# Kernel optimization log

Hardware: AMD Instinct MI355X
Metric: run time of the kernel (lower is better)

## Reference

```python
import jax, jax.numpy as jnp
import numpy as np

NR, NS, GS, APP_DIM = 4096, 128, 128, 27
FEAPE, VIEWPE, FC = 6, 6, 128
IN_MLPC = APP_DIM + 3 + 2 * FEAPE * APP_DIM + 2 * VIEWPE * 3  # 390
DENSITY_SHIFT, DIST_SCALE = -10.0, 25.0


def positional_encoding(x, freqs):
    # matches torch: (x[..., None] * 2**k).reshape(..., freqs*dim), then [sin, cos]
    fb = 2.0 ** jnp.arange(freqs, dtype=x.dtype)
    p = (x[..., None] * fb).reshape(x.shape[:-1] + (freqs * x.shape[-1],))
    return jnp.concatenate([jnp.sin(p), jnp.cos(p)], axis=-1)


def grid_sample3d(vol, coords):
    # vol: [C, D, H, W]; coords: [N, 3] xyz in [-1, 1] (x->W, y->H, z->D)
    # trilinear, align_corners=True (matches F.grid_sample)
    C, D, H, W = vol.shape

    def axis(c, S):
        i = (c + 1.0) * 0.5 * (S - 1)
        i0 = jnp.clip(jnp.floor(i), 0, S - 2).astype(jnp.int32)
        return i0, i - i0

    x0, wx = axis(coords[:, 0], W)
    y0, wy = axis(coords[:, 1], H)
    z0, wz = axis(coords[:, 2], D)

    def g(zi, yi, xi):
        return vol[:, zi, yi, xi]  # [C, N]

    c00 = g(z0, y0, x0) * (1 - wx) + g(z0, y0, x0 + 1) * wx
    c01 = g(z0, y0 + 1, x0) * (1 - wx) + g(z0, y0 + 1, x0 + 1) * wx
    c10 = g(z0 + 1, y0, x0) * (1 - wx) + g(z0 + 1, y0, x0 + 1) * wx
    c11 = g(z0 + 1, y0 + 1, x0) * (1 - wx) + g(z0 + 1, y0 + 1, x0 + 1) * wx
    c0 = c00 * (1 - wy) + c01 * wy
    c1 = c10 * (1 - wy) + c11 * wy
    return (c0 * (1 - wz) + c1 * wz).T  # [N, C]


def setup_inputs() -> dict:
    key = jax.random.key(0)
    ks = jax.random.split(key, 12)
    xyz = jax.random.uniform(ks[0], (NR, NS, 3), jnp.float32, -1.0, 1.0)
    viewdirs = jax.random.normal(ks[1], (NR, 3), jnp.float32)
    viewdirs = viewdirs / jnp.linalg.norm(viewdirs, axis=-1, keepdims=True)
    dists = jax.random.uniform(ks[2], (NR, NS), jnp.float32, 0.0, 0.02)
    density_grid = jax.random.normal(ks[3], (1, GS, GS, GS), jnp.float32) * 3.0 + 8.0
    app_grid = jax.random.normal(ks[4], (APP_DIM, GS, GS, GS), jnp.float32) * 0.1
    w1 = jax.random.normal(ks[5], (IN_MLPC, FC), jnp.float32) / np.sqrt(IN_MLPC)
    b1 = jnp.zeros((FC,), jnp.float32)
    w2 = jax.random.normal(ks[6], (FC, FC), jnp.float32) / np.sqrt(FC)
    b2 = jnp.zeros((FC,), jnp.float32)
    w3 = jax.random.normal(ks[7], (FC, 3), jnp.float32) / np.sqrt(FC)
    b3 = jnp.zeros((3,), jnp.float32)
    return {"xyz": xyz, "viewdirs": viewdirs, "dists": dists,
            "density_grid": density_grid, "app_grid": app_grid,
            "w1": w1, "b1": b1, "w2": w2, "b2": b2, "w3": w3, "b3": b3}


def reference(xyz, viewdirs, dists, density_grid, app_grid, w1, b1, w2, b2, w3, b3):
    nr, ns, _ = xyz.shape
    pts = xyz.reshape(-1, 3)

    # density feature lookup + softplus feature2density (fea2denseAct='softplus')
    sigma_feat = grid_sample3d(density_grid, pts)[:, 0].reshape(nr, ns)
    sigma = jax.nn.softplus(sigma_feat + DENSITY_SHIFT)

    # raw2alpha: alpha compositing with transmittance cumprod
    alpha = 1.0 - jnp.exp(-sigma * dists * DIST_SCALE)  # [nr, ns]
    T = jnp.cumprod(jnp.concatenate(
        [jnp.ones((nr, 1), alpha.dtype), 1.0 - alpha + 1e-10], axis=-1), axis=-1)
    weights = alpha * T[:, :-1]  # [nr, ns]

    # appearance feature lookup + MLPRender_Fea shading
    feats = grid_sample3d(app_grid, pts)  # [nr*ns, 27]
    vdirs = jnp.broadcast_to(viewdirs[:, None, :], (nr, ns, 3)).reshape(-1, 3)
    mlp_in = jnp.concatenate(
        [feats, vdirs,
         positional_encoding(feats, FEAPE),
         positional_encoding(vdirs, VIEWPE)], axis=-1)  # [nr*ns, 390]
    h = jax.nn.relu(mlp_in @ w1 + b1)
    h = jax.nn.relu(h @ w2 + b2)
    rgb = jax.nn.sigmoid(h @ w3 + b3).reshape(nr, ns, 3)

    rgb_map = jnp.sum(weights[..., None] * rgb, axis=1)  # [nr, 3]
    return rgb_map
```

## Files before the change

kernel.cpp:

```cpp
#include <hip/hip_runtime.h>
#include <math.h>

#define NRAYS  4096
#define NSAMP  128
#define GSZ    128
#define VOX    (GSZ*GSZ*GSZ)
#define APPC   27
#define FCH    128
#define INW    390
#define K1PAD  416
#define TP     32
#define SIP    424
#define H1S    136
#define H2S    132
#define VOXPAD 32

typedef __attribute__((ext_vector_type(8))) short bf16x8;
typedef __attribute__((ext_vector_type(4))) float f32x4;

#define MFMA16(a, b, c) __builtin_amdgcn_mfma_f32_16x16x32_bf16((a), (b), (c), 0, 0, 0)

__device__ inline ushort f2b(float f) {
    union { float f; unsigned u; } x; x.f = f;
    unsigned u = x.u;
    u = (u + 0x7FFFu + ((u >> 16) & 1u)) >> 16;
    return (ushort)u;
}
__device__ inline float b2f(ushort h) {
    return __uint_as_float(((unsigned)h) << 16);
}

__global__ __launch_bounds__(256)
void transpose_app(const float* __restrict__ ag, ushort* __restrict__ out)
{
    const int v = blockIdx.x * 256 + threadIdx.x;
    ushort h[VOXPAD];
    #pragma unroll
    for (int c = 0; c < APPC; c++)
        h[c] = f2b(ag[(size_t)c * VOX + v]);
    #pragma unroll
    for (int c = APPC; c < VOXPAD; c++) h[c] = 0;
    uint4* o = reinterpret_cast<uint4*>(out + (size_t)v * VOXPAD);
    #pragma unroll
    for (int i = 0; i < 4; i++) {
        uint4 q;
        q.x = (unsigned)h[8*i+0] | ((unsigned)h[8*i+1] << 16);
        q.y = (unsigned)h[8*i+2] | ((unsigned)h[8*i+3] << 16);
        q.z = (unsigned)h[8*i+4] | ((unsigned)h[8*i+5] << 16);
        q.w = (unsigned)h[8*i+6] | ((unsigned)h[8*i+7] << 16);
        o[i] = q;
    }
}

__device__ inline bf16x8 load_b_frag(const float* __restrict__ W, int ld,
                                     int kbase, int n, int kmax)
{
    union { uint4 u; bf16x8 v; } cv;
    unsigned* pr = &cv.u.x;
    #pragma unroll
    for (int q = 0; q < 4; q++) {
        const int ka = kbase + 2*q, kb = ka + 1;
        const float fa = (ka < kmax) ? W[ka*ld + n] : 0.f;
        const float fb = (kb < kmax) ? W[kb*ld + n] : 0.f;
        pr[q] = (unsigned)f2b(fa) | ((unsigned)f2b(fb) << 16);
    }
    return cv.v;
}

__global__ __launch_bounds__(256)
void nerf_render_mfma(const float* __restrict__ xyz,
                      const float* __restrict__ viewdirs,
                      const float* __restrict__ dists,
                      const float* __restrict__ dgrid,
                      const ushort* __restrict__ agridT,
                      const float* __restrict__ w1,
                      const float* __restrict__ b1,
                      const float* __restrict__ w2,
                      const float* __restrict__ b2,
                      const float* __restrict__ w3,
                      const float* __restrict__ b3,
                      float* __restrict__ out)
{
    __shared__ __align__(16) ushort S_in[TP][SIP];
    __shared__ __align__(16) ushort s_h1[TP][H1S];
    __shared__ float  s_h2[TP][H2S];
    __shared__ int    s_base[NSAMP];
    __shared__ float  s_w8[NSAMP][8];
    __shared__ float  s_wts[NSAMP];
    __shared__ ushort s_vrow[40];
    __shared__ float  s_partial[TP*3];
    __shared__ float  s_scanw0;

    const int r    = blockIdx.x;
    const int t    = threadIdx.x;
    const int lane = t & 63;

    for (int i = t; i < TP*SIP/2; i += 256)
        reinterpret_cast<unsigned*>(&S_in[0][0])[i] = 0u;
    if (t < TP*3) s_partial[t] = 0.f;

    {
        const int s = t & 127;
        const float px = xyz[(r*NSAMP + s)*3 + 0];
        const float py = xyz[(r*NSAMP + s)*3 + 1];
        const float pz = xyz[(r*NSAMP + s)*3 + 2];
        float fx = (px + 1.0f) * 63.5f;
        float fy = (py + 1.0f) * 63.5f;
        float fz = (pz + 1.0f) * 63.5f;
        int x0 = (int)floorf(fx); x0 = min(max(x0, 0), GSZ-2);
        int y0 = (int)floorf(fy); y0 = min(max(y0, 0), GSZ-2);
        int z0 = (int)floorf(fz); z0 = min(max(z0, 0), GSZ-2);
        float wx = fx - (float)x0, wy = fy - (float)y0, wz = fz - (float)z0;
        float ux = 1.f - wx, uy = 1.f - wy, uz = 1.f - wz;
        int base = (z0*GSZ + y0)*GSZ + x0;
        float w000 = uz*uy*ux, w001 = uz*uy*wx, w010 = uz*wy*ux, w011 = uz*wy*wx;
        float w100 = wz*uy*ux, w101 = wz*uy*wx, w110 = wz*wy*ux, w111 = wz*wy*wx;
        if (t < 128) {
            s_base[s] = base;
            s_w8[s][0] = w000; s_w8[s][1] = w001; s_w8[s][2] = w010; s_w8[s][3] = w011;
            s_w8[s][4] = w100; s_w8[s][5] = w101; s_w8[s][6] = w110; s_w8[s][7] = w111;
        }
        const float* dg = dgrid + base;
        float dsum = w000*dg[0]            + w001*dg[1]
                   + w010*dg[GSZ]          + w011*dg[GSZ+1]
                   + w100*dg[GSZ*GSZ]      + w101*dg[GSZ*GSZ+1]
                   + w110*dg[GSZ*GSZ+GSZ]  + w111*dg[GSZ*GSZ+GSZ+1];
        float sf    = dsum - 10.0f;
        float sigma = fmaxf(sf, 0.f) + log1pf(expf(-fabsf(sf)));
        float alpha = 1.f - expf(-sigma * dists[r*NSAMP + s] * 25.0f);
        float v     = 1.f - alpha + 1e-10f;

        float scan = v;
        #pragma unroll
        for (int off = 1; off < 64; off <<= 1) {
            float o = __shfl_up(scan, off, 64);
            if (lane >= off) scan *= o;
        }
        if ((t & 127) == 63) s_scanw0 = scan;
        __syncthreads();
        float prev = __shfl_up(scan, 1, 64);
        float excl;
        if ((t & 127) < 64) excl = (lane == 0) ? 1.0f     : prev;
        else                excl = (lane == 0) ? s_scanw0 : prev * s_scanw0;
        if (t < 128) s_wts[s] = alpha * excl;
    }

    if (t < 21) {
        if (t < 3) {
            s_vrow[t] = f2b(viewdirs[r*3 + t]);
        } else {
            int i = t - 3;
            int d = i / 6, f = i - 6*d;
            float vd = viewdirs[r*3 + d];
            float sv, cv;
            sincosf(vd * (float)(1 << f), &sv, &cv);
            s_vrow[3  + i] = f2b(sv);
            s_vrow[21 + i] = f2b(cv);
        }
    }
    __syncthreads();

    for (int s0 = 0; s0 < NSAMP; s0 += TP) {
        {
            const int p   = t >> 3;
            const int tap = t & 7;
            const int s   = s0 + p;
            const int dz  = tap >> 2, dy = (tap >> 1) & 1, dx = tap & 1;
            const int vox = s_base[s] + dz*GSZ*GSZ + dy*GSZ + dx;
            const float wt = s_w8[s][tap];
            const ushort* vp = agridT + (size_t)vox * VOXPAD;
            const uint4 a0 = *reinterpret_cast<const uint4*>(vp);
            const uint4 a1 = *reinterpret_cast<const uint4*>(vp + 8);
            const uint4 a2 = *reinterpret_cast<const uint4*>(vp + 16);
            const uint2 a3 = *reinterpret_cast<const uint2*>(vp + 24);
            unsigned dw[14] = {a0.x,a0.y,a0.z,a0.w, a1.x,a1.y,a1.z,a1.w,
                               a2.x,a2.y,a2.z,a2.w, a3.x,a3.y};
            float f[27];
            #pragma unroll
            for (int i = 0; i < 14; i++) {
                f[2*i] = __uint_as_float(dw[i] << 16) * wt;
                if (2*i + 1 < 27)
                    f[2*i+1] = __uint_as_float(dw[i] & 0xffff0000u) * wt;
            }
            #pragma unroll
            for (int m = 1; m < 8; m <<= 1) {
                #pragma unroll
                for (int c = 0; c < 27; c++)
                    f[c] += __shfl_xor(f[c], m, 64);
            }
            #pragma unroll
            for (int c = 0; c < APPC; c++)
                if ((c & 7) == tap) S_in[p][c] = f2b(f[c]);
        }
        for (int idx = t; idx < TP*39; idx += 256) {
            int p = idx / 39, j = idx - p*39;
            S_in[p][(j < 3) ? (27 + j) : (351 + j)] = s_vrow[j];
        }
        __syncthreads();

        for (int idx = t; idx < TP*162; idx += 256) {
            int p   = idx / 162;
            int rem = idx - p*162;
            int d = rem / 6, f = rem - 6*d;
            float v = b2f(S_in[p][d]);
            float sv, cv;
            __sincosf(v * (float)(1 << f), &sv, &cv);
            S_in[p][30  + rem] = f2b(sv);
            S_in[p][192 + rem] = f2b(cv);
        }
        __syncthreads();

        const int wv = t >> 6;
        const int mt = wv & 1, nq = wv >> 1;
        const int arow  = mt*16 + (lane & 15);
        const int kg    = (lane >> 4) * 8;
        const int ncol  = lane & 15;
        const int mbase = mt*16 + (lane >> 4)*4;

        {
            f32x4 acc0 = {0.f,0.f,0.f,0.f}, acc1 = {0.f,0.f,0.f,0.f};
            f32x4 acc2 = {0.f,0.f,0.f,0.f}, acc3 = {0.f,0.f,0.f,0.f};
            const int n0 = (nq*4+0)*16 + ncol, n1 = (nq*4+1)*16 + ncol;
            const int n2 = (nq*4+2)*16 + ncol, n3 = (nq*4+3)*16 + ncol;
            for (int ks = 0; ks < 13; ks++) {
                const int k0 = ks*32 + kg;
                bf16x8 a = *reinterpret_cast<const bf16x8*>(&S_in[arow][k0]);
                acc0 = MFMA16(a, load_b_frag(w1, FCH, k0, n0, INW), acc0);
                acc1 = MFMA16(a, load_b_frag(w1, FCH, k0, n1, INW), acc1);
                acc2 = MFMA16(a, load_b_frag(w1, FCH, k0, n2, INW), acc2);
                acc3 = MFMA16(a, load_b_frag(w1, FCH, k0, n3, INW), acc3);
            }
            const float bn0 = b1[n0], bn1 = b1[n1], bn2 = b1[n2], bn3 = b1[n3];
            #pragma unroll
            for (int q = 0; q < 4; q++) {
                s_h1[mbase + q][n0] = f2b(fmaxf(acc0[q] + bn0, 0.f));
                s_h1[mbase + q][n1] = f2b(fmaxf(acc1[q] + bn1, 0.f));
                s_h1[mbase + q][n2] = f2b(fmaxf(acc2[q] + bn2, 0.f));
                s_h1[mbase + q][n3] = f2b(fmaxf(acc3[q] + bn3, 0.f));
            }
        }
        __syncthreads();

        {
            f32x4 acc0 = {0.f,0.f,0.f,0.f}, acc1 = {0.f,0.f,0.f,0.f};
            f32x4 acc2 = {0.f,0.f,0.f,0.f}, acc3 = {0.f,0.f,0.f,0.f};
            const int n0 = (nq*4+0)*16 + ncol, n1 = (nq*4+1)*16 + ncol;
            const int n2 = (nq*4+2)*16 + ncol, n3 = (nq*4+3)*16 + ncol;
            #pragma unroll
            for (int ks = 0; ks < 4; ks++) {
                const int k0 = ks*32 + kg;
                bf16x8 a = *reinterpret_cast<const bf16x8*>(&s_h1[arow][k0]);
                acc0 = MFMA16(a, load_b_frag(w2, FCH, k0, n0, FCH), acc0);
                acc1 = MFMA16(a, load_b_frag(w2, FCH, k0, n1, FCH), acc1);
                acc2 = MFMA16(a, load_b_frag(w2, FCH, k0, n2, FCH), acc2);
                acc3 = MFMA16(a, load_b_frag(w2, FCH, k0, n3, FCH), acc3);
            }
            const float bn0 = b2[n0], bn1 = b2[n1], bn2 = b2[n2], bn3 = b2[n3];
            #pragma unroll
            for (int q = 0; q < 4; q++) {
                s_h2[mbase + q][n0] = fmaxf(acc0[q] + bn0, 0.f);
                s_h2[mbase + q][n1] = fmaxf(acc1[q] + bn1, 0.f);
                s_h2[mbase + q][n2] = fmaxf(acc2[q] + bn2, 0.f);
                s_h2[mbase + q][n3] = fmaxf(acc3[q] + bn3, 0.f);
            }
        }
        __syncthreads();

        if (t < TP*3) {
            int p = t / 3, c = t - 3*p;
            float acc = b3[c];
            for (int k = 0; k < FCH; k++)
                acc = fmaf(s_h2[p][k], w3[k*3 + c], acc);
            float rgb = 1.0f / (1.0f + expf(-acc));
            s_partial[t] += s_wts[s0 + p] * rgb;
        }
        __syncthreads();
    }

    if (t < 3) {
        float sum = 0.f;
        #pragma unroll
        for (int p = 0; p < TP; p++) sum += s_partial[p*3 + t];
        out[r*3 + t] = sum;
    }
}

__global__ __launch_bounds__(128)
void nerf_render_f32(const float* __restrict__ xyz,
                     const float* __restrict__ viewdirs,
                     const float* __restrict__ dists,
                     const float* __restrict__ dgrid,
                     const float* __restrict__ agrid,
                     const float* __restrict__ w1,
                     const float* __restrict__ b1,
                     const float* __restrict__ w2,
                     const float* __restrict__ b2,
                     const float* __restrict__ w3,
                     const float* __restrict__ b3,
                     float* __restrict__ out)
{
    __shared__ int   s_base[NSAMP];
    __shared__ float s_w8[NSAMP][8];
    __shared__ float s_wts[NSAMP];
    __shared__ float s_vrow[40];
    __shared__ float S_in[16][392];
    __shared__ float s_h1[16][FCH];
    __shared__ float s_partial[16*3];
    __shared__ float s_scanw0;
    float (* const s_h2)[FCH] = reinterpret_cast<float (*)[FCH]>(&S_in[0][0]);

    const int r = blockIdx.x, t = threadIdx.x, lane = t & 63;
    if (t < 48) s_partial[t] = 0.f;
    {
        const int s = t;
        const float px = xyz[(r*NSAMP + s)*3 + 0];
        const float py = xyz[(r*NSAMP + s)*3 + 1];
        const float pz = xyz[(r*NSAMP + s)*3 + 2];
        float fx = (px + 1.0f) * 63.5f, fy = (py + 1.0f) * 63.5f, fz = (pz + 1.0f) * 63.5f;
        int x0 = (int)floorf(fx); x0 = min(max(x0, 0), GSZ-2);
        int y0 = (int)floorf(fy); y0 = min(max(y0, 0), GSZ-2);
        int z0 = (int)floorf(fz); z0 = min(max(z0, 0), GSZ-2);
        float wx = fx - x0, wy = fy - y0, wz = fz - z0;
        float ux = 1.f - wx, uy = 1.f - wy, uz = 1.f - wz;
        int base = (z0*GSZ + y0)*GSZ + x0;
        s_base[s] = base;
        float w000 = uz*uy*ux, w001 = uz*uy*wx, w010 = uz*wy*ux, w011 = uz*wy*wx;
        float w100 = wz*uy*ux, w101 = wz*uy*wx, w110 = wz*wy*ux, w111 = wz*wy*wx;
        s_w8[s][0]=w000; s_w8[s][1]=w001; s_w8[s][2]=w010; s_w8[s][3]=w011;
        s_w8[s][4]=w100; s_w8[s][5]=w101; s_w8[s][6]=w110; s_w8[s][7]=w111;
        const float* dg = dgrid + base;
        float dsum = w000*dg[0]+w001*dg[1]+w010*dg[GSZ]+w011*dg[GSZ+1]
                   + w100*dg[GSZ*GSZ]+w101*dg[GSZ*GSZ+1]
                   + w110*dg[GSZ*GSZ+GSZ]+w111*dg[GSZ*GSZ+GSZ+1];
        float sf = dsum - 10.0f;
        float sigma = fmaxf(sf, 0.f) + log1pf(expf(-fabsf(sf)));
        float alpha = 1.f - expf(-sigma * dists[r*NSAMP + s] * 25.0f);
        float v = 1.f - alpha + 1e-10f;
        float scan = v;
        #pragma unroll
        for (int off = 1; off < 64; off <<= 1) {
            float o = __shfl_up(scan, off, 64);
            if (lane >= off) scan *= o;
        }
        if (t == 63) s_scanw0 = scan;
        __syncthreads();
        float prev = __shfl_up(scan, 1, 64);
        float excl;
        if (t < 64) excl = (lane == 0) ? 1.0f : prev;
        else        excl = (lane == 0) ? s_scanw0 : prev * s_scanw0;
        s_wts[s] = alpha * excl;
    }
    if (t < 21) {
        if (t < 3) s_vrow[t] = viewdirs[r*3 + t];
        else {
            int i = t - 3, d = i / 6, f = i - 6*d;
            float sv, cv;
            sincosf(viewdirs[r*3 + d] * (float)(1 << f), &sv, &cv);
            s_vrow[3 + i] = sv; s_vrow[21 + i] = cv;
        }
    }
    __syncthreads();
    for (int s0 = 0; s0 < NSAMP; s0 += 16) {
        for (int idx = t; idx < 16*APPC; idx += 128) {
            int p = idx / APPC, c = idx - p*APPC, s = s0 + p;
            const float* ag = agrid + (size_t)c*VOX + s_base[s];
            const float* w8 = s_w8[s];
            S_in[p][c] = w8[0]*ag[0]+w8[1]*ag[1]+w8[2]*ag[GSZ]+w8[3]*ag[GSZ+1]
                       + w8[4]*ag[GSZ*GSZ]+w8[5]*ag[GSZ*GSZ+1]
                       + w8[6]*ag[GSZ*GSZ+GSZ]+w8[7]*ag[GSZ*GSZ+GSZ+1];
        }
        for (int idx = t; idx < 16*39; idx += 128) {
            int p = idx / 39, j = idx - p*39;
            S_in[p][(j < 3) ? (27 + j) : (351 + j)] = s_vrow[j];
        }
        __syncthreads();
        for (int idx = t; idx < 16*162; idx += 128) {
            int p = idx / 162, rem = idx - p*162;
            int d = rem / 6, f = rem - 6*d;
            float sv, cv;
            __sincosf(S_in[p][d] * (float)(1 << f), &sv, &cv);
            S_in[p][30 + rem] = sv; S_in[p][192 + rem] = cv;
        }
        __syncthreads();
        {
            const int j = t; float acc[16]; const float bj = b1[j];
            #pragma unroll
            for (int p = 0; p < 16; p++) acc[p] = bj;
            for (int k = 0; k < INW; k += 2) {
                float wk0 = w1[k*FCH + j], wk1 = w1[(k+1)*FCH + j];
                #pragma unroll
                for (int p = 0; p < 16; p++)
                    acc[p] = fmaf(S_in[p][k+1], wk1, fmaf(S_in[p][k], wk0, acc[p]));
            }
            #pragma unroll
            for (int p = 0; p < 16; p++) s_h1[p][j] = fmaxf(acc[p], 0.f);
        }
        __syncthreads();
        {
            const int j = t; float acc[16]; const float bj = b2[j];
            #pragma unroll
            for (int p = 0; p < 16; p++) acc[p] = bj;
            for (int k = 0; k < FCH; k += 2) {
                float wk0 = w2[k*FCH + j], wk1 = w2[(k+1)*FCH + j];
                #pragma unroll
                for (int p = 0; p < 16; p++)
                    acc[p] = fmaf(s_h1[p][k+1], wk1, fmaf(s_h1[p][k], wk0, acc[p]));
            }
            #pragma unroll
            for (int p = 0; p < 16; p++) s_h2[p][j] = fmaxf(acc[p], 0.f);
        }
        __syncthreads();
        if (t < 48) {
            int p = t / 3, c = t - 3*p;
            float acc = b3[c];
            for (int k = 0; k < FCH; k++) acc = fmaf(s_h2[p][k], w3[k*3 + c], acc);
            s_partial[t] += s_wts[s0 + p] / (1.0f + expf(-acc));
        }
        __syncthreads();
    }
    if (t < 3) {
        float sum = 0.f;
        #pragma unroll
        for (int p = 0; p < 16; p++) sum += s_partial[p*3 + t];
        out[r*3 + t] = sum;
    }
}

extern "C" void kernel_launch(void* const* d_in, const int* in_sizes, int n_in,
                              void* d_out, int out_size, void* d_ws, size_t ws_size,
                              hipStream_t stream) {
    const float* xyz      = (const float*)d_in[0];
    const float* viewdirs = (const float*)d_in[1];
    const float* dists    = (const float*)d_in[2];
    const float* dgrid    = (const float*)d_in[3];
    const float* agrid    = (const float*)d_in[4];
    const float* w1       = (const float*)d_in[5];
    const float* b1       = (const float*)d_in[6];
    const float* w2       = (const float*)d_in[7];
    const float* b2       = (const float*)d_in[8];
    const float* w3       = (const float*)d_in[9];
    const float* b3       = (const float*)d_in[10];
    float* out = (float*)d_out;

    const size_t need = (size_t)VOX * VOXPAD * sizeof(ushort);
    if (ws_size >= need) {
        ushort* agT = (ushort*)d_ws;
        hipLaunchKernelGGL(transpose_app, dim3(VOX/256), dim3(256), 0, stream,
                           agrid, agT);
        hipLaunchKernelGGL(nerf_render_mfma, dim3(NRAYS), dim3(256), 0, stream,
                           xyz, viewdirs, dists, dgrid, agT,
                           w1, b1, w2, b2, w3, b3, out);
    } else {
        hipLaunchKernelGGL(nerf_render_f32, dim3(NRAYS), dim3(128), 0, stream,
                           xyz, viewdirs, dists, dgrid, agrid,
                           w1, b1, w2, b2, w3, b3, out);
    }
}
```

Baseline: 1.210 ms.

## Prepack MLP weights into bf16 MFMA fragment layout and shrink shared memory

Adds a prepack kernel that converts w1/w2 to bf16 once, already arranged in MFMA B-fragment order. Each lane then loads one 16-byte vector per MFMA instead of doing eight strided fp32 loads and conversions per fragment. It also aliases the layer-2 output buffer onto the input staging buffer, shrinks its padding, and raises the launch bound to 4 blocks per CU to improve occupancy. The transpose kernel now stages through LDS so its global stores are coalesced. The padding columns are re-zeroed on each sample tile because the aliased buffer overwrites them; this adds an extra kernel launch and some workspace use.

```diff
diff --git a/kernel.cpp b/kernel.cpp
--- a/kernel.cpp
+++ b/kernel.cpp
@@ -8,12 +8,13 @@
 #define APPC   27
 #define FCH    128
 #define INW    390
-#define K1PAD  416
 #define TP     32
-#define SIP    424
+#define SIP    416
 #define H1S    136
 #define H2S    132
 #define VOXPAD 32
+#define W1FR   (13*8*64*8)
+#define W2FR   (4*8*64*8)
 
 typedef __attribute__((ext_vector_type(8))) short bf16x8;
 typedef __attribute__((ext_vector_type(4))) float f32x4;
@@ -33,23 +34,52 @@
 __global__ __launch_bounds__(256)
 void transpose_app(const float* __restrict__ ag, ushort* __restrict__ out)
 {
-    const int v = blockIdx.x * 256 + threadIdx.x;
-    ushort h[VOXPAD];
+    __shared__ __align__(16) ushort ls[256][40];
+    const int t  = threadIdx.x;
+    const int v0 = blockIdx.x * 256;
+    const int v  = v0 + t;
     #pragma unroll
     for (int c = 0; c < APPC; c++)
-        h[c] = f2b(ag[(size_t)c * VOX + v]);
+        ls[t][c] = f2b(ag[(size_t)c * VOX + v]);
     #pragma unroll
-    for (int c = APPC; c < VOXPAD; c++) h[c] = 0;
-    uint4* o = reinterpret_cast<uint4*>(out + (size_t)v * VOXPAD);
+    for (int c = APPC; c < VOXPAD; c++) ls[t][c] = 0;
+    __syncthreads();
+    uint4* o4 = reinterpret_cast<uint4*>(out + (size_t)v0 * VOXPAD);
     #pragma unroll
     for (int i = 0; i < 4; i++) {
-        uint4 q;
-        q.x = (unsigned)h[8*i+0] | ((unsigned)h[8*i+1] << 16);
-        q.y = (unsigned)h[8*i+2] | ((unsigned)h[8*i+3] << 16);
-        q.z = (unsigned)h[8*i+4] | ((unsigned)h[8*i+5] << 16);
-        q.w = (unsigned)h[8*i+6] | ((unsigned)h[8*i+7] << 16);
-        o[i] = q;
-    }
+        const int j  = i*256 + t;
+        const int vv = j >> 2, i2 = j & 3;
+        o4[j] = *reinterpret_cast<const uint4*>(&ls[vv][i2*8]);
+    }
+}
+
+__global__ __launch_bounds__(256)
+void prepack_w(const float* __restrict__ w1, const float* __restrict__ w2,
+               ushort* __restrict__ w1p, ushort* __restrict__ w2p)
+{
+    int tid = blockIdx.x*256 + threadIdx.x;
+    const float* W; ushort* P; int kmax, ks, nt, lane;
+    if (tid < 13*8*64) {
+        W = w1; P = w1p; kmax = INW;
+        lane = tid & 63; nt = (tid >> 6) & 7; ks = tid >> 9;
+    } else {
+        int t2 = tid - 13*8*64;
+        if (t2 >= 4*8*64) return;
+        W = w2; P = w2p; kmax = FCH;
+        lane = t2 & 63; nt = (t2 >> 6) & 7; ks = t2 >> 9;
+    }
+    const int n  = nt*16 + (lane & 15);
+    const int k0 = ks*32 + (lane >> 4)*8;
+    unsigned d[4];
+    #pragma unroll
+    for (int q = 0; q < 4; q++) {
+        const int ka = k0 + 2*q, kb = ka + 1;
+        const float fa = (ka < kmax) ? W[ka*FCH + n] : 0.f;
+        const float fb = (kb < kmax) ? W[kb*FCH + n] : 0.f;
+        d[q] = (unsigned)f2b(fa) | ((unsigned)f2b(fb) << 16);
+    }
+    uint4* o = reinterpret_cast<uint4*>(P + ((size_t)((ks*8 + nt)*64 + lane)) * 8);
+    *o = make_uint4(d[0], d[1], d[2], d[3]);
 }
 
 __device__ inline bf16x8 load_b_frag(const float* __restrict__ W, int ld,
@@ -67,12 +97,15 @@
     return cv.v;
 }
 
-__global__ __launch_bounds__(256)
+template<bool PACKED>
+__global__ __launch_bounds__(256, 4)
 void nerf_render_mfma(const float* __restrict__ xyz,
                       const float* __restrict__ viewdirs,
                       const float* __restrict__ dists,
                       const float* __restrict__ dgrid,
                       const ushort* __restrict__ agridT,
+                      const ushort* __restrict__ w1p,
+                      const ushort* __restrict__ w2p,
                       const float* __restrict__ w1,
                       const float* __restrict__ b1,
                       const float* __restrict__ w2,
@@ -83,13 +116,14 @@
 {
     __shared__ __align__(16) ushort S_in[TP][SIP];
     __shared__ __align__(16) ushort s_h1[TP][H1S];
-    __shared__ float  s_h2[TP][H2S];
     __shared__ int    s_base[NSAMP];
     __shared__ float  s_w8[NSAMP][8];
     __shared__ float  s_wts[NSAMP];
     __shared__ ushort s_vrow[40];
     __shared__ float  s_partial[TP*3];
     __shared__ float  s_scanw0;
+
+    float* const s_h2f = reinterpret_cast<float*>(&S_in[0][0]);
 
     const int r    = blockIdx.x;
     const int t    = threadIdx.x;
@@ -161,6 +195,10 @@
     __syncthreads();
 
     for (int s0 = 0; s0 < NSAMP; s0 += TP) {
+        for (int idx = t; idx < TP*13; idx += 256) {
+            int row = idx / 13, d = idx - row*13;
+            reinterpret_cast<unsigned*>(&S_in[row][390])[d] = 0u;
+        }
         {
             const int p   = t >> 3;
             const int tap = t & 7;
@@ -225,10 +263,18 @@
             for (int ks = 0; ks < 13; ks++) {
                 const int k0 = ks*32 + kg;
                 bf16x8 a = *reinterpret_cast<const bf16x8*>(&S_in[arow][k0]);
-                acc0 = MFMA16(a, load_b_frag(w1, FCH, k0, n0, INW), acc0);
-                acc1 = MFMA16(a, load_b_frag(w1, FCH, k0, n1, INW), acc1);
-                acc2 = MFMA16(a, load_b_frag(w1, FCH, k0, n2, INW), acc2);
-                acc3 = MFMA16(a, load_b_frag(w1, FCH, k0, n3, INW), acc3);
+                if (PACKED) {
+                    const ushort* bp = w1p + ((size_t)(ks*8 + nq*4)*64 + lane)*8;
+                    acc0 = MFMA16(a, *reinterpret_cast<const bf16x8*>(bp),         acc0);
+                    acc1 = MFMA16(a, *reinterpret_cast<const bf16x8*>(bp + 512),   acc1);
+                    acc2 = MFMA16(a, *reinterpret_cast<const bf16x8*>(bp + 1024),  acc2);
+                    acc3 = MFMA16(a, *reinterpret_cast<const bf16x8*>(bp + 1536),  acc3);
+                } else {
+                    acc0 = MFMA16(a, load_b_frag(w1, FCH, k0, n0, INW), acc0);
+                    acc1 = MFMA16(a, load_b_frag(w1, FCH, k0, n1, INW), acc1);
+                    acc2 = MFMA16(a, load_b_frag(w1, FCH, k0, n2, INW), acc2);
+                    acc3 = MFMA16(a, load_b_frag(w1, FCH, k0, n3, INW), acc3);
+                }
             }
             const float bn0 = b1[n0], bn1 = b1[n1], bn2 = b1[n2], bn3 = b1[n3];
             #pragma unroll
@@ -250,18 +296,26 @@
             for (int ks = 0; ks < 4; ks++) {
                 const int k0 = ks*32 + kg;
                 bf16x8 a = *reinterpret_cast<const bf16x8*>(&s_h1[arow][k0]);
-                acc0 = MFMA16(a, load_b_frag(w2, FCH, k0, n0, FCH), acc0);
-                acc1 = MFMA16(a, load_b_frag(w2, FCH, k0, n1, FCH), acc1);
-                acc2 = MFMA16(a, load_b_frag(w2, FCH, k0, n2, FCH), acc2);
-                acc3 = MFMA16(a, load_b_frag(w2, FCH, k0, n3, FCH), acc3);
+                if (PACKED) {
+                    const ushort* bp = w2p + ((size_t)(ks*8 + nq*4)*64 + lane)*8;
+                    acc0 = MFMA16(a, *reinterpret_cast<const bf16x8*>(bp),         acc0);
+                    acc1 = MFMA16(a, *reinterpret_cast<const bf16x8*>(bp + 512),   acc1);
+                    acc2 = MFMA16(a, *reinterpret_cast<const bf16x8*>(bp + 1024),  acc2);
+                    acc3 = MFMA16(a, *reinterpret_cast<const bf16x8*>(bp + 1536),  acc3);
+                } else {
+                    acc0 = MFMA16(a, load_b_frag(w2, FCH, k0, n0, FCH), acc0);
+                    acc1 = MFMA16(a, load_b_frag(w2, FCH, k0, n1, FCH), acc1);
+                    acc2 = MFMA16(a, load_b_frag(w2, FCH, k0, n2, FCH), acc2);
+                    acc3 = MFMA16(a, load_b_frag(w2, FCH, k0, n3, FCH), acc3);
+                }
             }
             const float bn0 = b2[n0], bn1 = b2[n1], bn2 = b2[n2], bn3 = b2[n3];
             #pragma unroll
             for (int q = 0; q < 4; q++) {
-                s_h2[mbase + q][n0] = fmaxf(acc0[q] + bn0, 0.f);
-                s_h2[mbase + q][n1] = fmaxf(acc1[q] + bn1, 0.f);
-                s_h2[mbase + q][n2] = fmaxf(acc2[q] + bn2, 0.f);
-                s_h2[mbase + q][n3] = fmaxf(acc3[q] + bn3, 0.f);
+                s_h2f[(mbase + q)*H2S + n0] = fmaxf(acc0[q] + bn0, 0.f);
+                s_h2f[(mbase + q)*H2S + n1] = fmaxf(acc1[q] + bn1, 0.f);
+                s_h2f[(mbase + q)*H2S + n2] = fmaxf(acc2[q] + bn2, 0.f);
+                s_h2f[(mbase + q)*H2S + n3] = fmaxf(acc3[q] + bn3, 0.f);
             }
         }
         __syncthreads();
@@ -270,7 +324,7 @@
             int p = t / 3, c = t - 3*p;
             float acc = b3[c];
             for (int k = 0; k < FCH; k++)
-                acc = fmaf(s_h2[p][k], w3[k*3 + c], acc);
+                acc = fmaf(s_h2f[p*H2S + k], w3[k*3 + c], acc);
             float rgb = 1.0f / (1.0f + expf(-acc));
             s_partial[t] += s_wts[s0 + p] * rgb;
         }
@@ -442,14 +496,26 @@
     const float* b3       = (const float*)d_in[10];
     float* out = (float*)d_out;
 
-    const size_t need = (size_t)VOX * VOXPAD * sizeof(ushort);
-    if (ws_size >= need) {
+    const size_t needT = (size_t)VOX * VOXPAD * sizeof(ushort);
+    const size_t needP = needT + (size_t)(W1FR + W2FR) * sizeof(ushort);
+
+    if (ws_size >= needT) {
         ushort* agT = (ushort*)d_ws;
         hipLaunchKernelGGL(transpose_app, dim3(VOX/256), dim3(256), 0, stream,
                            agrid, agT);
-        hipLaunchKernelGGL(nerf_render_mfma, dim3(NRAYS), dim3(256), 0, stream,
-                           xyz, viewdirs, dists, dgrid, agT,
-                           w1, b1, w2, b2, w3, b3, out);
+        if (ws_size >= needP) {
+            ushort* w1p = agT + (size_t)VOX * VOXPAD;
+            ushort* w2p = w1p + W1FR;
+            hipLaunchKernelGGL(prepack_w, dim3(34), dim3(256), 0, stream,
+                               w1, w2, w1p, w2p);
+            hipLaunchKernelGGL((nerf_render_mfma<true>), dim3(NRAYS), dim3(256), 0, stream,
+                               xyz, viewdirs, dists, dgrid, agT, w1p, w2p,
+                               w1, b1, w2, b2, w3, b3, out);
+        } else {
+            hipLaunchKernelGGL((nerf_render_mfma<false>), dim3(NRAYS), dim3(256), 0, stream,
+                               xyz, viewdirs, dists, dgrid, agT, agT, agT,
+                               w1, b1, w2, b2, w3, b3, out);
+        }
     } else {
         hipLaunchKernelGGL(nerf_render_f32, dim3(NRAYS), dim3(128), 0, stream,
                            xyz, viewdirs, dists, dgrid, agrid,
```

New measurement: 1.628 ms. +34.6%, slower.
